# Kernel tuning notes

Measured on AMD Instinct MI355X. Metric: run time of the kernel, lower is better.

## Reference

```python
import jax, jax.numpy as jnp
import numpy as np

E = 1024; H = 16; HD = E // H; T = 2048; B = 2; TOPK = E  # top_r = 1.0 -> top_k = out_features


def _dgl(x, lw, lb, g, b, w1, b1, w2, b2):
    """DGLLayer: x (l, n, c) -> (l, n, out). Top-k gated linear projection.
    Equivalent to the torch per-sample gather/matmul/scatter loop, vectorized:
    out[i, o, t] = (x @ lw.T + lb)[i, t, o] if o in topk indices of sample i else 0.
    """
    xn = jnp.transpose(x, (1, 0, 2))              # (n, l, c)
    xa = jnp.mean(xn, axis=1)                     # (n, c)  avg_pool1d over length
    mu = jnp.mean(xa, axis=-1, keepdims=True)     # LayerNorm
    var = jnp.mean((xa - mu) ** 2, axis=-1, keepdims=True)
    hn = (xa - mu) * jax.lax.rsqrt(var + 1e-5) * g + b
    logits = hn @ lw.T + lb                       # gate predictor input (linear with l_w)
    logits = jax.nn.relu(logits @ w1.T + b1)      # MLP
    logits = jax.nn.relu(logits @ w2.T + b2)
    idx = jax.lax.top_k(logits, TOPK)[1]          # (n, k)
    n = xn.shape[0]
    mask = jnp.zeros((n, lw.shape[0]), x.dtype).at[jnp.arange(n)[:, None], idx].set(1.0)
    out = (xn @ lw.T + lb) * mask[:, None, :]     # (n, l, out); zeros outside top-k
    return jnp.transpose(out, (1, 0, 2))          # (l, n, out)


def setup_inputs() -> dict:
    rng = jax.random.key(0)
    ks = jax.random.split(rng, 11)
    s = 0.02
    return {
        "query": jax.random.normal(ks[0], (T, B, E), jnp.float32),
        "key": jax.random.normal(ks[1], (T, B, E), jnp.float32),
        "value": jax.random.normal(ks[2], (T, B, E), jnp.float32),
        "in_proj_w": jax.random.normal(ks[3], (3 * E, E), jnp.float32) * s,
        "in_proj_b": jax.random.normal(ks[4], (3 * E,), jnp.float32) * s,
        "out_w": jax.random.normal(ks[5], (E, E), jnp.float32) * s,
        "out_b": jax.random.normal(ks[6], (E,), jnp.float32) * s,
        # per-DGL-layer params stacked: index 0=q, 1=k, 2=v, 3=out
        "ln_g": jnp.ones((4, E), jnp.float32),
        "ln_b": jnp.zeros((4, E), jnp.float32),
        "gw1": jax.random.normal(ks[7], (4, E, E), jnp.float32) * s,
        "gb1": jax.random.normal(ks[8], (4, E), jnp.float32) * s,
        "gw2": jax.random.normal(ks[9], (4, E, E), jnp.float32) * s,
        "gb2": jax.random.normal(ks[10], (4, E), jnp.float32) * s,
    }


def reference(query, key, value, in_proj_w, in_proj_b, out_w, out_b,
              ln_g, ln_b, gw1, gb1, gw2, gb2):
    wq, wk, wv = jnp.split(in_proj_w, 3, axis=0)
    bq, bk, bv = jnp.split(in_proj_b, 3, axis=0)
    q = _dgl(query, wq, bq, ln_g[0], ln_b[0], gw1[0], gb1[0], gw2[0], gb2[0])
    k = _dgl(key, wk, bk, ln_g[1], ln_b[1], gw1[1], gb1[1], gw2[1], gb2[1])
    v = _dgl(value, wv, bv, ln_g[2], ln_b[2], gw1[2], gb1[2], gw2[2], gb2[2])
    # (T, B, E) -> (B*H, T, HD)
    q = jnp.swapaxes(q.reshape(T, B * H, HD), 0, 1)
    k = jnp.swapaxes(k.reshape(T, B * H, HD), 0, 1)
    v = jnp.swapaxes(v.reshape(T, B * H, HD), 0, 1)
    scores = jnp.einsum('bte,bse->bts', q / np.float32(np.sqrt(HD)), k)
    attn = jax.nn.softmax(scores, axis=-1)        # (B*H, T, T)
    ao = jnp.einsum('bts,bse->bte', attn, v)
    ao = jnp.swapaxes(ao, 0, 1).reshape(T * B, E)  # (tgt*bsz, E)
    # out DGL layer sees a 2-D input -> treated as n=1, l=tgt*bsz (one global gate)
    ao = _dgl(ao[:, None, :], out_w, out_b, ln_g[3], ln_b[3], gw1[3], gb1[3], gw2[3], gb2[3])
    attn_output = ao.reshape(T, B, E)
    attn_weights = attn.reshape(B, H, T, T).mean(axis=1)  # average_attn_weights=True
    return (attn_output, attn_weights)
```

## Files before the change

### kernel.cpp

```cpp
#include <hip/hip_runtime.h>
#include <hip/hip_bf16.h>
#include <cstdint>
#include <cstddef>

#define T_DIM 2048
#define B_DIM 2
#define E_DIM 1024
#define H_DIM 16
#define HD_DIM 64
#define M_ROWS 4096
#define BH_DIM 32

typedef __attribute__((ext_vector_type(8))) short bf16x8;
typedef __attribute__((ext_vector_type(4))) float f32x4;

__device__ __forceinline__ short f2bf(float x) {
  unsigned u = __float_as_uint(x);
  u += 0x7fffu + ((u >> 16) & 1u);
  return (short)(u >> 16);
}

__device__ __forceinline__ float exp2_hw(float x) {
  return __builtin_amdgcn_exp2f(x);
}

__device__ __forceinline__ f32x4 mfma_bf16(bf16x8 a, bf16x8 b, f32x4 c) {
  return __builtin_amdgcn_mfma_f32_16x16x32_bf16(a, b, c, 0, 0, 0);
}

__device__ __forceinline__ unsigned cvt_pk_bf16(float lo, float hi) {
  unsigned r;
  asm volatile("v_cvt_pk_bf16_f32 %0, %1, %2" : "=v"(r) : "v"(lo), "v"(hi));
  return r;
}

__device__ __forceinline__ void gload_lds16(const void* g, void* l) {
  __builtin_amdgcn_global_load_lds(
      (const __attribute__((address_space(1))) void*)g,
      (__attribute__((address_space(3))) void*)l,
      16, 0, 0);
}

__global__ __launch_bounds__(256) void cvt_bf16_kernel(const float* __restrict__ src,
                                                       short* __restrict__ dst, int n4) {
  int i = blockIdx.x * blockDim.x + threadIdx.x;
  if (i < n4) {
    float4 v = ((const float4*)src)[i];
    short4 o;
    o.x = f2bf(v.x); o.y = f2bf(v.y); o.z = f2bf(v.z); o.w = f2bf(v.w);
    ((short4*)dst)[i] = o;
  }
}

__global__ __launch_bounds__(256) void proj_gemm_kernel(
    const short* __restrict__ A0, const short* __restrict__ W0,
    const float* __restrict__ b0,
    short* __restrict__ q_s, short* __restrict__ k_s, short* __restrict__ vT,
    float* __restrict__ outf, int mode_in) {
  int mode = (mode_in < 0) ? (int)blockIdx.z : mode_in;
  const short* A = (mode_in < 0) ? A0 + (size_t)mode * (size_t)M_ROWS * 1024 : A0;
  const short* W = W0 + (size_t)mode * 1024 * 1024;
  const float* bias = (mode_in < 0) ? b0 + mode * 1024 : b0;

  __shared__ short As[128 * 32];
  __shared__ short Bs[128 * 32];

  int tid = threadIdx.x;
  int lane = tid & 63;
  int wave = tid >> 6;
  int wm = wave >> 1, wn = wave & 1;
  int brow = blockIdx.y * 128;
  int bcol = blockIdx.x * 128;

  f32x4 acc[4][4];
#pragma unroll
  for (int i = 0; i < 4; i++)
#pragma unroll
    for (int j = 0; j < 4; j++) acc[i][j] = (f32x4){0.f, 0.f, 0.f, 0.f};

  for (int k0 = 0; k0 < 1024; k0 += 32) {
#pragma unroll
    for (int j = 0; j < 2; j++) {
      int chunk = wave * 2 + j;
      int row = chunk * 16 + (lane >> 2);
      int col = (lane & 3) * 8;
      gload_lds16(A + (size_t)(brow + row) * 1024 + k0 + col, &As[chunk * 512]);
      gload_lds16(W + (size_t)(bcol + row) * 1024 + k0 + col, &Bs[chunk * 512]);
    }
    __syncthreads();

    bf16x8 af[4], bf_[4];
#pragma unroll
    for (int mi = 0; mi < 4; mi++)
      af[mi] = *(const bf16x8*)&As[(wm * 64 + mi * 16 + (lane & 15)) * 32 + (lane >> 4) * 8];
#pragma unroll
    for (int ni = 0; ni < 4; ni++)
      bf_[ni] = *(const bf16x8*)&Bs[(wn * 64 + ni * 16 + (lane & 15)) * 32 + (lane >> 4) * 8];
#pragma unroll
    for (int mi = 0; mi < 4; mi++)
#pragma unroll
      for (int ni = 0; ni < 4; ni++)
        acc[mi][ni] = mfma_bf16(af[mi], bf_[ni], acc[mi][ni]);
    __syncthreads();
  }

#pragma unroll
  for (int mi = 0; mi < 4; mi++) {
#pragma unroll
    for (int ni = 0; ni < 4; ni++) {
      int col = bcol + wn * 64 + ni * 16 + (lane & 15);
      float bv = bias[col];
      int row0 = brow + wm * 64 + mi * 16 + (lane >> 4) * 4;
#pragma unroll
      for (int r = 0; r < 4; r++) {
        int row = row0 + r;
        float val = acc[mi][ni][r] + bv;
        int t = row >> 1, b = row & 1;
        int h = col >> 6, hd = col & 63;
        if (mode == 0) {
          q_s[((size_t)((b << 4) + h) * T_DIM + t) * HD_DIM + hd] =
              f2bf(val * 0.1803368801f);
        } else if (mode == 1) {
          k_s[((size_t)((b << 4) + h) * T_DIM + t) * HD_DIM + hd] = f2bf(val);
        } else if (mode == 2) {
          vT[((size_t)((b << 4) + h) * HD_DIM + hd) * T_DIM + t] = f2bf(val);
        } else {
          outf[(size_t)row * 1024 + col] = val;
        }
      }
    }
  }
}

__device__ __forceinline__ void stage_kv(const short* kb, const short* vb, int s0,
                                         short* Ktb, short* Vtb, int tid) {
  int r0 = tid >> 3;
  int sx = (tid & 7) ^ (r0 & 7);
  gload_lds16(kb + (size_t)(s0 + r0) * 64 + sx * 8, Ktb + tid * 8);
  gload_lds16(kb + (size_t)(s0 + 32 + r0) * 64 + sx * 8, Ktb + 2048 + tid * 8);
  gload_lds16(vb + (size_t)r0 * T_DIM + s0 + sx * 8, Vtb + tid * 8);
  gload_lds16(vb + (size_t)(32 + r0) * T_DIM + s0 + sx * 8, Vtb + 2048 + tid * 8);
}

__global__ __launch_bounds__(256) void flash_fwd_kernel(
    const short* __restrict__ q_s, const short* __restrict__ k_s,
    const short* __restrict__ vT, short* __restrict__ AO,
    float* __restrict__ c_ws) {
  int bh = blockIdx.y;
  int tid = threadIdx.x;
  int lane = tid & 63;
  int wave = tid >> 6;
  int t0w = blockIdx.x * 128 + wave * 32;
  int tp = lane & 15;
  int g = lane >> 4;
  int sw = tp & 7;

  const short* qb = q_s + (size_t)bh * T_DIM * HD_DIM;
  const short* kb = k_s + (size_t)bh * T_DIM * HD_DIM;
  const short* vb = vT + (size_t)bh * HD_DIM * T_DIM;

  __shared__ short Kt[2][64 * 64];
  __shared__ short Vt[2][64 * 64];
  __shared__ short Pt[4][2][16 * 72];

  bf16x8 qfA0 = *(const bf16x8*)&qb[(t0w + tp) * HD_DIM + g * 8];
  bf16x8 qfA1 = *(const bf16x8*)&qb[(t0w + tp) * HD_DIM + 32 + g * 8];
  bf16x8 qfB0 = *(const bf16x8*)&qb[(t0w + 16 + tp) * HD_DIM + g * 8];
  bf16x8 qfB1 = *(const bf16x8*)&qb[(t0w + 16 + tp) * HD_DIM + 32 + g * 8];

  f32x4 accA[4], accB[4];
#pragma unroll
  for (int i = 0; i < 4; i++) {
    accA[i] = (f32x4){0.f, 0.f, 0.f, 0.f};
    accB[i] = (f32x4){0.f, 0.f, 0.f, 0.f};
  }
  float lA = 0.f, lB = 0.f;

  short* PA = Pt[wave][0];
  short* PB = Pt[wave][1];

  stage_kv(kb, vb, 0, Kt[0], Vt[0], tid);

#pragma unroll 1
  for (int i = 0; i < 32; ++i) {
    int cur = i & 1;
    __syncthreads();
    if (i + 1 < 32) stage_kv(kb, vb, (i + 1) * 64, Kt[cur ^ 1], Vt[cur ^ 1], tid);
    const short* Kc = Kt[cur];
    const short* Vc = Vt[cur];

#pragma unroll
    for (int sn = 0; sn < 4; ++sn) {
      int row = sn * 16 + tp;
      bf16x8 kf0 = *(const bf16x8*)&Kc[row * 64 + (g ^ sw) * 8];
      bf16x8 kf1 = *(const bf16x8*)&Kc[row * 64 + ((g | 4) ^ sw) * 8];
      f32x4 zA = (f32x4){0.f, 0.f, 0.f, 0.f};
      zA = mfma_bf16(kf0, qfA0, zA);
      zA = mfma_bf16(kf1, qfA1, zA);
      f32x4 zB = (f32x4){0.f, 0.f, 0.f, 0.f};
      zB = mfma_bf16(kf0, qfB0, zB);
      zB = mfma_bf16(kf1, qfB1, zB);
      float a0 = exp2_hw(zA[0]), a1 = exp2_hw(zA[1]);
      float a2 = exp2_hw(zA[2]), a3 = exp2_hw(zA[3]);
      float b0 = exp2_hw(zB[0]), b1 = exp2_hw(zB[1]);
      float b2 = exp2_hw(zB[2]), b3 = exp2_hw(zB[3]);
      lA += (a0 + a1) + (a2 + a3);
      lB += (b0 + b1) + (b2 + b3);
      uint2 wa, wb;
      wa.x = cvt_pk_bf16(a0, a1); wa.y = cvt_pk_bf16(a2, a3);
      wb.x = cvt_pk_bf16(b0, b1); wb.y = cvt_pk_bf16(b2, b3);
      *(uint2*)&PA[tp * 72 + sn * 16 + g * 4] = wa;
      *(uint2*)&PB[tp * 72 + sn * 16 + g * 4] = wb;
    }

#pragma unroll
    for (int c32 = 0; c32 < 2; ++c32) {
      bf16x8 pfA = *(const bf16x8*)&PA[tp * 72 + c32 * 32 + g * 8];
      bf16x8 pfB = *(const bf16x8*)&PB[tp * 72 + c32 * 32 + g * 8];
#pragma unroll
      for (int hdt = 0; hdt < 4; ++hdt) {
        bf16x8 vf = *(const bf16x8*)&Vc[(hdt * 16 + tp) * 64 + ((c32 * 4 + g) ^ sw) * 8];
        accA[hdt] = mfma_bf16(pfA, vf, accA[hdt]);
        accB[hdt] = mfma_bf16(pfB, vf, accB[hdt]);
      }
    }
  }

  lA += __shfl_xor(lA, 16); lA += __shfl_xor(lA, 32);
  lB += __shfl_xor(lB, 16); lB += __shfl_xor(lB, 32);
  float liA[4], liB[4];
#pragma unroll
  for (int r = 0; r < 4; r++) {
    liA[r] = 1.0f / __shfl(lA, g * 4 + r);
    liB[r] = 1.0f / __shfl(lB, g * 4 + r);
  }
  int b = bh >> 4, h = bh & 15;
#pragma unroll
  for (int hdt = 0; hdt < 4; hdt++) {
#pragma unroll
    for (int r = 0; r < 4; r++) {
      int tA = t0w + g * 4 + r;
      int tB = t0w + 16 + g * 4 + r;
      AO[(size_t)(tA * 2 + b) * E_DIM + h * 64 + hdt * 16 + tp] =
          f2bf(accA[hdt][r] * liA[r]);
      AO[(size_t)(tB * 2 + b) * E_DIM + h * 64 + hdt * 16 + tp] =
          f2bf(accB[hdt][r] * liB[r]);
    }
  }
  if (lane < 16) {
    c_ws[bh * T_DIM + t0w + tp] = -__log2f(lA);
    c_ws[bh * T_DIM + t0w + 16 + tp] = -__log2f(lB);
  }
}

__device__ __forceinline__ void stage_qk(const short* qh, const short* kh,
                                         int tbase, int sbase,
                                         short* Qb, short* Kb, int tid) {
  int r0 = tid >> 3;
  int sx = (tid & 7) ^ (r0 & 7);
  gload_lds16(qh + (size_t)(tbase + r0) * 64 + sx * 8, Qb + tid * 8);
  gload_lds16(qh + (size_t)(tbase + 32 + r0) * 64 + sx * 8, Qb + 2048 + tid * 8);
  gload_lds16(kh + (size_t)(sbase + r0) * 64 + sx * 8, Kb + tid * 8);
  gload_lds16(kh + (size_t)(sbase + 32 + r0) * 64 + sx * 8, Kb + 2048 + tid * 8);
}

__global__ __launch_bounds__(256) void attn_weights_kernel(
    const short* __restrict__ q_s, const short* __restrict__ k_s,
    const float* __restrict__ c_ws, float* __restrict__ wout) {
  int b = blockIdx.z;
  int tid = threadIdx.x;
  int lane = tid & 63;
  int wave = tid >> 6;
  int tbase = blockIdx.y * 64;
  int sbase = blockIdx.x * 64;
  int tp = lane & 15;
  int g = lane >> 4;
  int tw = wave * 16;
  int tq = tbase + tw + g * 4;
  int sw = tp & 7;

  __shared__ short Qt[2][64 * 64];
  __shared__ short Kt[2][64 * 64];

  float wsum[4][4];
#pragma unroll
  for (int st = 0; st < 4; st++)
#pragma unroll
    for (int r = 0; r < 4; r++) wsum[st][r] = 0.f;

  const size_t hstride = (size_t)T_DIM * HD_DIM;
  const short* qh0 = q_s + (size_t)(b * 16) * hstride;
  const short* kh0 = k_s + (size_t)(b * 16) * hstride;

  stage_qk(qh0, kh0, tbase, sbase, Qt[0], Kt[0], tid);

#pragma unroll 1
  for (int h = 0; h < 16; ++h) {
    int bh = b * 16 + h;
    int cur = h & 1;
    float4 cc = *(const float4*)&c_ws[(size_t)bh * T_DIM + tq];
    __syncthreads();
    if (h + 1 < 16)
      stage_qk(qh0 + (size_t)(h + 1) * hstride, kh0 + (size_t)(h + 1) * hstride,
               tbase, sbase, Qt[cur ^ 1], Kt[cur ^ 1], tid);
    const short* Qc = Qt[cur];
    const short* Kc = Kt[cur];

    bf16x8 qf0 = *(const bf16x8*)&Qc[(tw + tp) * 64 + (g ^ sw) * 8];
    bf16x8 qf1 = *(const bf16x8*)&Qc[(tw + tp) * 64 + ((g | 4) ^ sw) * 8];
#pragma unroll
    for (int st = 0; st < 4; ++st) {
      int row = st * 16 + tp;
      bf16x8 kf0 = *(const bf16x8*)&Kc[row * 64 + (g ^ sw) * 8];
      bf16x8 kf1 = *(const bf16x8*)&Kc[row * 64 + ((g | 4) ^ sw) * 8];
      f32x4 z = (f32x4){0.f, 0.f, 0.f, 0.f};
      z = mfma_bf16(qf0, kf0, z);
      z = mfma_bf16(qf1, kf1, z);
      wsum[st][0] += exp2_hw(z[0] + cc.x);
      wsum[st][1] += exp2_hw(z[1] + cc.y);
      wsum[st][2] += exp2_hw(z[2] + cc.z);
      wsum[st][3] += exp2_hw(z[3] + cc.w);
    }
  }

#pragma unroll
  for (int st = 0; st < 4; st++)
#pragma unroll
    for (int r = 0; r < 4; r++)
      wout[((size_t)b * T_DIM + tq + r) * T_DIM + sbase + st * 16 + tp] =
          wsum[st][r] * 0.0625f;
}

extern "C" void kernel_launch(void* const* d_in, const int* in_sizes, int n_in,
                              void* d_out, int out_size, void* d_ws, size_t ws_size,
                              hipStream_t stream) {
  const float* query = (const float*)d_in[0];
  const float* key = (const float*)d_in[1];
  const float* value = (const float*)d_in[2];
  const float* in_proj_w = (const float*)d_in[3];
  const float* in_proj_b = (const float*)d_in[4];
  const float* out_w = (const float*)d_in[5];
  const float* out_b = (const float*)d_in[6];

  float* out = (float*)d_out;
  float* wout = out + (size_t)M_ROWS * E_DIM;

  char* ws = (char*)d_ws;
  short* Wb = (short*)ws;
  short* Xb = (short*)(ws + (8ull << 20));
  short* q_s = (short*)(ws + (32ull << 20));
  short* k_s = (short*)(ws + (40ull << 20));
  short* vT = (short*)(ws + (48ull << 20));
  short* AO = (short*)(ws + (56ull << 20));
  float* c_ws = (float*)(ws + (64ull << 20));

  cvt_bf16_kernel<<<4096, 256, 0, stream>>>(query, Xb, 1048576);
  cvt_bf16_kernel<<<4096, 256, 0, stream>>>(key, Xb + 4194304, 1048576);
  cvt_bf16_kernel<<<4096, 256, 0, stream>>>(value, Xb + 8388608, 1048576);
  cvt_bf16_kernel<<<3072, 256, 0, stream>>>(in_proj_w, Wb, 786432);
  cvt_bf16_kernel<<<1024, 256, 0, stream>>>(out_w, Wb + 3145728, 262144);

  proj_gemm_kernel<<<dim3(8, 32, 3), 256, 0, stream>>>(
      Xb, Wb, in_proj_b, q_s, k_s, vT, nullptr, -1);

  flash_fwd_kernel<<<dim3(16, 32), 256, 0, stream>>>(q_s, k_s, vT, AO, c_ws);

  attn_weights_kernel<<<dim3(32, 32, 2), 256, 0, stream>>>(q_s, k_s, c_ws, wout);

  proj_gemm_kernel<<<dim3(8, 32, 1), 256, 0, stream>>>(
      AO, Wb, out_b, nullptr, nullptr, nullptr, out, 3);
}
```

Before: 192.4 us.

## Double query tile in attn-weights kernel and overlap staged loads with raw barriers

In the attn-weights kernel, each block now covers 128 query rows instead of 64, so every staged K tile feeds two MFMA tiles per wave and the grid halves. In both the flash and attn-weights loops, __syncthreads is replaced by explicit s_barrier pairs with partial vmcnt waits, so the prefetch of the next tile can stay in flight while the current one is consumed. The cost is more LDS for Q, more registers for the doubled accumulators, and a dependence on the hand-set vmcnt counts matching the number of async loads issued.

```diff
diff --git a/kernel.cpp b/kernel.cpp
--- a/kernel.cpp
+++ b/kernel.cpp
@@ -184,8 +184,15 @@
 #pragma unroll 1
   for (int i = 0; i < 32; ++i) {
     int cur = i & 1;
-    __syncthreads();
-    if (i + 1 < 32) stage_kv(kb, vb, (i + 1) * 64, Kt[cur ^ 1], Vt[cur ^ 1], tid);
+    __builtin_amdgcn_s_barrier();
+    if (i + 1 < 32) {
+      stage_kv(kb, vb, (i + 1) * 64, Kt[cur ^ 1], Vt[cur ^ 1], tid);
+      asm volatile("s_waitcnt vmcnt(4)" ::: "memory");
+    } else {
+      asm volatile("s_waitcnt vmcnt(0)" ::: "memory");
+    }
+    __builtin_amdgcn_s_barrier();
+    __builtin_amdgcn_sched_barrier(0);
     const short* Kc = Kt[cur];
     const short* Vc = Vt[cur];
 
@@ -258,8 +265,10 @@
                                          short* Qb, short* Kb, int tid) {
   int r0 = tid >> 3;
   int sx = (tid & 7) ^ (r0 & 7);
-  gload_lds16(qh + (size_t)(tbase + r0) * 64 + sx * 8, Qb + tid * 8);
-  gload_lds16(qh + (size_t)(tbase + 32 + r0) * 64 + sx * 8, Qb + 2048 + tid * 8);
+#pragma unroll
+  for (int c = 0; c < 4; ++c)
+    gload_lds16(qh + (size_t)(tbase + c * 32 + r0) * 64 + sx * 8,
+                Qb + c * 2048 + tid * 8);
   gload_lds16(kh + (size_t)(sbase + r0) * 64 + sx * 8, Kb + tid * 8);
   gload_lds16(kh + (size_t)(sbase + 32 + r0) * 64 + sx * 8, Kb + 2048 + tid * 8);
 }
@@ -271,22 +280,23 @@
   int tid = threadIdx.x;
   int lane = tid & 63;
   int wave = tid >> 6;
-  int tbase = blockIdx.y * 64;
+  int tbase = blockIdx.y * 128;
   int sbase = blockIdx.x * 64;
   int tp = lane & 15;
   int g = lane >> 4;
-  int tw = wave * 16;
-  int tq = tbase + tw + g * 4;
+  int tw = wave * 32;
+  int tqA = tbase + tw + g * 4;
+  int tqB = tqA + 16;
   int sw = tp & 7;
 
-  __shared__ short Qt[2][64 * 64];
+  __shared__ short Qt[2][128 * 64];
   __shared__ short Kt[2][64 * 64];
 
-  float wsum[4][4];
+  float wsA[4][4], wsB[4][4];
 #pragma unroll
   for (int st = 0; st < 4; st++)
 #pragma unroll
-    for (int r = 0; r < 4; r++) wsum[st][r] = 0.f;
+    for (int r = 0; r < 4; r++) { wsA[st][r] = 0.f; wsB[st][r] = 0.f; }
 
   const size_t hstride = (size_t)T_DIM * HD_DIM;
   const short* qh0 = q_s + (size_t)(b * 16) * hstride;
@@ -298,37 +308,56 @@
   for (int h = 0; h < 16; ++h) {
     int bh = b * 16 + h;
     int cur = h & 1;
-    float4 cc = *(const float4*)&c_ws[(size_t)bh * T_DIM + tq];
-    __syncthreads();
-    if (h + 1 < 16)
+    float4 ccA = *(const float4*)&c_ws[(size_t)bh * T_DIM + tqA];
+    float4 ccB = *(const float4*)&c_ws[(size_t)bh * T_DIM + tqB];
+    __builtin_amdgcn_s_barrier();
+    if (h + 1 < 16) {
       stage_qk(qh0 + (size_t)(h + 1) * hstride, kh0 + (size_t)(h + 1) * hstride,
                tbase, sbase, Qt[cur ^ 1], Kt[cur ^ 1], tid);
+      asm volatile("s_waitcnt vmcnt(6)" ::: "memory");
+    } else {
+      asm volatile("s_waitcnt vmcnt(0)" ::: "memory");
+    }
+    __builtin_amdgcn_s_barrier();
+    __builtin_amdgcn_sched_barrier(0);
     const short* Qc = Qt[cur];
     const short* Kc = Kt[cur];
 
-    bf16x8 qf0 = *(const bf16x8*)&Qc[(tw + tp) * 64 + (g ^ sw) * 8];
-    bf16x8 qf1 = *(const bf16x8*)&Qc[(tw + tp) * 64 + ((g | 4) ^ sw) * 8];
+    bf16x8 qfA0 = *(const bf16x8*)&Qc[(tw + tp) * 64 + (g ^ sw) * 8];
+    bf16x8 qfA1 = *(const bf16x8*)&Qc[(tw + tp) * 64 + ((g | 4) ^ sw) * 8];
+    bf16x8 qfB0 = *(const bf16x8*)&Qc[(tw + 16 + tp) * 64 + (g ^ sw) * 8];
+    bf16x8 qfB1 = *(const bf16x8*)&Qc[(tw + 16 + tp) * 64 + ((g | 4) ^ sw) * 8];
 #pragma unroll
     for (int st = 0; st < 4; ++st) {
       int row = st * 16 + tp;
       bf16x8 kf0 = *(const bf16x8*)&Kc[row * 64 + (g ^ sw) * 8];
       bf16x8 kf1 = *(const bf16x8*)&Kc[row * 64 + ((g | 4) ^ sw) * 8];
-      f32x4 z = (f32x4){0.f, 0.f, 0.f, 0.f};
-      z = mfma_bf16(qf0, kf0, z);
-      z = mfma_bf16(qf1, kf1, z);
-      wsum[st][0] += exp2_hw(z[0] + cc.x);
-      wsum[st][1] += exp2_hw(z[1] + cc.y);
-      wsum[st][2] += exp2_hw(z[2] + cc.z);
-      wsum[st][3] += exp2_hw(z[3] + cc.w);
+      f32x4 zA = (f32x4){0.f, 0.f, 0.f, 0.f};
+      zA = mfma_bf16(qfA0, kf0, zA);
+      zA = mfma_bf16(qfA1, kf1, zA);
+      f32x4 zB = (f32x4){0.f, 0.f, 0.f, 0.f};
+      zB = mfma_bf16(qfB0, kf0, zB);
+      zB = mfma_bf16(qfB1, kf1, zB);
+      wsA[st][0] += exp2_hw(zA[0] + ccA.x);
+      wsA[st][1] += exp2_hw(zA[1] + ccA.y);
+      wsA[st][2] += exp2_hw(zA[2] + ccA.z);
+      wsA[st][3] += exp2_hw(zA[3] + ccA.w);
+      wsB[st][0] += exp2_hw(zB[0] + ccB.x);
+      wsB[st][1] += exp2_hw(zB[1] + ccB.y);
+      wsB[st][2] += exp2_hw(zB[2] + ccB.z);
+      wsB[st][3] += exp2_hw(zB[3] + ccB.w);
     }
   }
 
 #pragma unroll
   for (int st = 0; st < 4; st++)
 #pragma unroll
-    for (int r = 0; r < 4; r++)
-      wout[((size_t)b * T_DIM + tq + r) * T_DIM + sbase + st * 16 + tp] =
-          wsum[st][r] * 0.0625f;
+    for (int r = 0; r < 4; r++) {
+      wout[((size_t)b * T_DIM + tqA + r) * T_DIM + sbase + st * 16 + tp] =
+          wsA[st][r] * 0.0625f;
+      wout[((size_t)b * T_DIM + tqB + r) * T_DIM + sbase + st * 16 + tp] =
+          wsB[st][r] * 0.0625f;
+    }
 }
 
 extern "C" void kernel_launch(void* const* d_in, const int* in_sizes, int n_in,
@@ -365,7 +394,7 @@
 
   flash_fwd_kernel<<<dim3(16, 32), 256, 0, stream>>>(q_s, k_s, vT, AO, c_ws);
 
-  attn_weights_kernel<<<dim3(32, 32, 2), 256, 0, stream>>>(q_s, k_s, c_ws, wout);
+  attn_weights_kernel<<<dim3(32, 16, 2), 256, 0, stream>>>(q_s, k_s, c_ws, wout);
 
   proj_gemm_kernel<<<dim3(8, 32, 1), 256, 0, stream>>>(
       AO, Wb, out_b, nullptr, nullptr, nullptr, out, 3);
```

Result: no change. 190.5 us (-1.0%).
